# Optimization experiments

Measured on AMD Instinct MI355X. Metric: run time of the kernel, lower is better.

The kernel has to match this reference:

```python
import jax, jax.numpy as jnp
import numpy as np

K = 8
EPS = 1e-8


def setup_inputs() -> dict:
    key = jax.random.key(0)
    tokens = jax.random.normal(key, (32, 1024, 256), dtype=jnp.float32)
    return {"tokens": tokens}


def reference(tokens) -> jnp.ndarray:
    # tokens: [B, N, D] -> adjacency [B, N, N] float32 (0/1), mutual kNN, no self-loops
    B, N, D = tokens.shape
    tn = tokens / (jnp.linalg.norm(tokens, axis=-1, keepdims=True) + EPS)
    sim = jnp.einsum('bnd,bmd->bnm', tn, tn)  # [B, N, N] cosine similarity
    # mask diagonal (add_self=False)
    diag = jnp.eye(N, dtype=bool)
    sim = jnp.where(diag[None, :, :], -jnp.inf, sim)
    k = min(K, N - 1)
    _, topk_idx = jax.lax.top_k(sim, k)  # [B, N, k]
    b_idx = jnp.arange(B)[:, None, None]
    r_idx = jnp.arange(N)[None, :, None]
    adj = jnp.zeros((B, N, N), dtype=bool).at[b_idx, r_idx, topk_idx].set(True)
    # mutual kNN: keep edge only if both directions selected
    adj = adj & jnp.swapaxes(adj, 1, 2)
    return adj.astype(jnp.float32)
```

## Files before the change

### kernel.cpp

```cpp
#include <hip/hip_runtime.h>
#include <math.h>
#include <stdint.h>

#define B_ 32
#define N_ 1024
#define D_ 256
#define K_ 8
#define CAND 12

typedef unsigned short u16;
typedef unsigned int u32;
typedef __attribute__((ext_vector_type(8))) short s16x8;
typedef __attribute__((ext_vector_type(16))) float f32x16;

__device__ inline void cp16(const void* g, void* l) {
    __builtin_amdgcn_global_load_lds((const __attribute__((address_space(1))) void*)g,
                                     (__attribute__((address_space(3))) void*)l, 16, 0, 0);
}

__device__ inline u16 f2bf(float f) {
    uint32_t u = __float_as_uint(f);
    return (u16)((u + 0x7fffu + ((u >> 16) & 1u)) >> 16);
}
__device__ inline u32 umax32(u32 a, u32 b) { return a > b ? a : b; }
__device__ inline u32 umin32(u32 a, u32 b) { return a < b ? a : b; }

__global__ __launch_bounds__(256) void prep_kernel(const float* __restrict__ tok,
                                                   double* __restrict__ invn,
                                                   u16* __restrict__ xhi) {
    const int tid = threadIdx.x;
    const int wave = tid >> 6, lane = tid & 63;
    const int row = blockIdx.x * 4 + wave;
    const float4 v = *reinterpret_cast<const float4*>(tok + (size_t)row * D_ + lane * 4);
    double s = (double)v.x * v.x + (double)v.y * v.y +
               (double)v.z * v.z + (double)v.w * v.w;
    #pragma unroll
    for (int off = 32; off > 0; off >>= 1) s += __shfl_xor(s, off, 64);
    const double inv = 1.0 / (sqrt(s) + 1e-8);
    if (lane == 0) invn[row] = inv;
    ushort4 h;
    h.x = f2bf((float)(v.x * inv));
    h.y = f2bf((float)(v.y * inv));
    h.z = f2bf((float)(v.z * inv));
    h.w = f2bf((float)(v.w * inv));
    *reinterpret_cast<ushort4*>(xhi + (size_t)row * D_ + lane * 4) = h;
}

__global__ __launch_bounds__(256, 4) void sim_topk_kernel(const u16* __restrict__ Xhi,
                                                          u32* __restrict__ candk,
                                                          int* __restrict__ candj) {
    __shared__ __align__(16) char smem[32768];
    u32* keysL = (u32*)smem;

    const int id    = blockIdx.x;
    const int chunk = id >> 3;
    const int b   = (id & 7) * 4 + (chunk >> 5);
    const int rem = chunk & 31;
    const int i0  = (rem >> 1) * 64;
    const int jh  = rem & 1;

    const int tid = threadIdx.x;
    const int w = tid >> 6, lane = tid & 63;
    const int mq = w >> 1, nq = w & 1;
    const int half = lane >> 5;
    const int il = lane & 31;

    const u16* XhiB = Xhi + (size_t)b * N_ * D_;

    const int srr = lane >> 3, spp = lane & 7;
    const int sgoff = (spp ^ srr) * 8;
    char* const wbase = smem + w * 8192;

    const int x7 = il & 7;
    int loff[4];
    #pragma unroll
    for (int ks = 0; ks < 4; ++ks) loff[ks] = il * 128 + (((ks * 2 + half) ^ x7) * 16);

    auto STAGE_A = [&](int kc, int bufn) {
        #pragma unroll
        for (int t = 0; t < 4; ++t)
            cp16(XhiB + (size_t)(i0 + mq * 32 + t * 8 + srr) * D_ + kc * 64 + sgoff,
                 wbase + bufn * 4096 + t * 1024);
    };
    auto STAGE_B = [&](int round, int bufn) {
        const int j0n = (jh * 8 + (round >> 2)) * 64;
        const int kcn = round & 3;
        #pragma unroll
        for (int t = 0; t < 4; ++t)
            cp16(XhiB + (size_t)(j0n + nq * 32 + t * 8 + srr) * D_ + kcn * 64 + sgoff,
                 wbase + bufn * 4096 + t * 1024);
    };

    s16x8 Ahf[4][4];
    STAGE_A(0, 0);
    STAGE_A(1, 1);
    #pragma unroll
    for (int kc = 0; kc < 4; ++kc) {
        asm volatile("s_waitcnt vmcnt(4)" ::: "memory");
        __builtin_amdgcn_sched_barrier(0);
        const char* ab = wbase + (kc & 1) * 4096;
        #pragma unroll
        for (int ks = 0; ks < 4; ++ks)
            Ahf[kc][ks] = *(const s16x8*)(ab + loff[ks]);
        asm volatile("s_waitcnt lgkmcnt(0)" ::: "memory");
        __builtin_amdgcn_sched_barrier(0);
        if (kc < 2) STAGE_A(kc + 2, kc & 1);
        else        STAGE_B(kc - 2, kc & 1);
    }

    const int diag_jt = i0 >> 6;
    u32 keys[CAND];
    #pragma unroll
    for (int c = 0; c < CAND; ++c) keys[c] = 0u;

    for (int lt = 0; lt < 8; ++lt) {
        const int jt = jh * 8 + lt;
        f32x16 acc;
        #pragma unroll
        for (int c = 0; c < 16; ++c) acc[c] = 0.0f;

        #pragma unroll
        for (int kc = 0; kc < 4; ++kc) {
            const int r = lt * 4 + kc;
            if (r < 31) asm volatile("s_waitcnt vmcnt(4)" ::: "memory");
            else        asm volatile("s_waitcnt vmcnt(0)" ::: "memory");
            __builtin_amdgcn_sched_barrier(0);
            const char* bb = wbase + (r & 1) * 4096;
            s16x8 bh[4];
            #pragma unroll
            for (int ks = 0; ks < 4; ++ks)
                bh[ks] = *(const s16x8*)(bb + loff[ks]);
            asm volatile("s_waitcnt lgkmcnt(0)" ::: "memory");
            __builtin_amdgcn_sched_barrier(0);
            if (r + 2 < 32) STAGE_B(r + 2, r & 1);
            #pragma unroll
            for (int ks = 0; ks < 4; ++ks)
                acc = __builtin_amdgcn_mfma_f32_32x32x16_bf16(bh[ks], Ahf[kc][ks], acc, 0, 0, 0);
        }

        const u32 codebase = (u32)(jt << 4);
        const bool diag = (jt == diag_jt) && (mq == nq);
        #pragma unroll
        for (int rg = 0; rg < 16; ++rg) {
            const u32 u = __float_as_uint(acc[rg]);
            const u32 mono = u ^ ((u32)(((int)u) >> 31) | 0x80000000u);
            u32 key = (mono & 0xFFFFFF00u) | (codebase + (u32)rg);
            if (diag && ((rg & 3) + 8 * (rg >> 2) + 4 * half == il)) key = 0u;
            u32 t = key;
            #pragma unroll
            for (int c = 0; c < CAND; ++c) {
                const u32 hi = umax32(keys[c], t);
                t = umin32(keys[c], t);
                keys[c] = hi;
            }
        }
    }

    __syncthreads();
    {
        const int r = mq * 32 + il;
        const int s = nq * 2 + half;
        u32* dst = keysL + (r * 4 + s) * CAND;
        #pragma unroll
        for (int c = 0; c < CAND; ++c) dst[c] = keys[c];
    }
    __syncthreads();

    if (tid < 64) {
        const u32* kl = keysL + tid * (4 * CAND);
        const size_t base = ((size_t)(b * N_ + i0 + tid) * 2 + jh) * CAND;
        int p0 = 0, p1 = 0, p2 = 0, p3 = 0;
        #pragma unroll
        for (int o = 0; o < CAND; ++o) {
            const u32 k0v = kl[p0];
            const u32 k1v = kl[CAND + p1];
            const u32 k2v = kl[2 * CAND + p2];
            const u32 k3v = kl[3 * CAND + p3];
            int bg = 0; u32 bv = k0v;
            if (k1v > bv) { bv = k1v; bg = 1; }
            if (k2v > bv) { bv = k2v; bg = 2; }
            if (k3v > bv) { bv = k3v; bg = 3; }
            const int code = (int)(bv & 0xFFu);
            const int jtv = code >> 4, rg = code & 15;
            candk[base + o] = bv;
            candj[base + o] = jtv * 64 + (bg >> 1) * 32 + (rg & 3) + 8 * (rg >> 2)
                              + 4 * (bg & 1);
            p0 += (bg == 0); p1 += (bg == 1); p2 += (bg == 2); p3 += (bg == 3);
        }
    }
}

__global__ __launch_bounds__(512) void merge_rescore_kernel(const u32* __restrict__ candk,
                                                            const int* __restrict__ candj,
                                                            const float* __restrict__ tok,
                                                            const double* __restrict__ invn,
                                                            int* __restrict__ topk) {
    __shared__ int    mj[32 * CAND];
    __shared__ double dv[32 * CAND];
    const int tid = threadIdx.x;

    const int id    = blockIdx.x;
    const int chunk = id >> 3;
    const int b     = (id & 7) * 4 + (chunk >> 5);
    const int i0    = (chunk & 31) * 32;
    const int R0    = b * N_ + i0;

    if (tid < 32) {
        const size_t base = (size_t)(R0 + tid) * 2 * CAND;
        int p0 = 0, p1 = 0;
        #pragma unroll
        for (int o = 0; o < CAND; ++o) {
            const u32 k0 = candk[base + p0];
            const u32 k1 = candk[base + CAND + p1];
            if (k0 >= k1) { mj[tid * CAND + o] = candj[base + p0];        ++p0; }
            else          { mj[tid * CAND + o] = candj[base + CAND + p1]; ++p1; }
        }
    }
    __syncthreads();

    {
        const int q = tid >> 2, ql = tid & 3;
        const int r = q >> 2;
        const float* qi = tok + (size_t)(R0 + r) * D_;
        const double di = invn[R0 + r];
        #pragma unroll 1
        for (int rr = 0; rr < 3; ++rr) {
            const int c = (q & 3) * 3 + rr;
            const int j = mj[r * CAND + c];
            const float* qj = tok + (size_t)(b * N_ + j) * D_;
            double s = 0.0;
            #pragma unroll 4
            for (int k = 0; k < 16; ++k) {
                const float4 x = *reinterpret_cast<const float4*>(qi + k * 16 + ql * 4);
                const float4 y = *reinterpret_cast<const float4*>(qj + k * 16 + ql * 4);
                s += (double)x.x * y.x + (double)x.y * y.y +
                     (double)x.z * y.z + (double)x.w * y.w;
            }
            s += __shfl_xor(s, 1, 64);
            s += __shfl_xor(s, 2, 64);
            if (ql == 0) dv[r * CAND + c] = s * di * invn[b * N_ + j];
        }
    }
    __syncthreads();

    if (tid < 32) {
        const int out_base = (R0 + tid) * K_;
        #pragma unroll 1
        for (int c = 0; c < CAND; ++c) {
            const double dc = dv[tid * CAND + c]; const int jc = mj[tid * CAND + c];
            int rank = 0;
            #pragma unroll 1
            for (int c2 = 0; c2 < CAND; ++c2) {
                if (c2 == c) continue;
                const double d2 = dv[tid * CAND + c2]; const int j2 = mj[tid * CAND + c2];
                if (d2 > dc || (d2 == dc && j2 < jc)) ++rank;
            }
            if (rank < K_) topk[out_base + rank] = jc;
        }
    }
}

__global__ __launch_bounds__(256) void mutual_kernel(const int* __restrict__ topk,
                                                     float* __restrict__ out) {
    const int gid = blockIdx.x * 256 + threadIdx.x;
    const int row = gid >> 3, s = gid & 7;
    const int j = topk[row * K_ + s];
    const int i = row & (N_ - 1);
    const int* tj = topk + ((row & ~(N_ - 1)) + j) * K_;
    bool m = false;
    #pragma unroll
    for (int u = 0; u < K_; ++u) m = m || (tj[u] == i);
    if (m) out[(size_t)row * N_ + j] = 1.0f;
}

extern "C" void kernel_launch(void* const* d_in, const int* in_sizes, int n_in,
                              void* d_out, int out_size, void* d_ws, size_t ws_size,
                              hipStream_t stream) {
    const float* tok = (const float*)d_in[0];
    float* out = (float*)d_out;
    double* invn = (double*)d_ws;
    int* topk = (int*)((char*)d_ws + (size_t)B_ * N_ * sizeof(double));
    u16* xhi = (u16*)d_out;
    u32* candk = (u32*)((char*)d_out + (size_t)32 * 1024 * 1024);
    int* candj = (int*)((char*)d_out + (size_t)35 * 1024 * 1024);

    prep_kernel<<<dim3(B_ * N_ / 4), 256, 0, stream>>>(tok, invn, xhi);
    sim_topk_kernel<<<dim3(1024), 256, 0, stream>>>(xhi, candk, candj);
    merge_rescore_kernel<<<dim3(B_ * N_ / 32), 512, 0, stream>>>(candk, candj, tok, invn, topk);
    hipMemsetAsync(d_out, 0, (size_t)B_ * N_ * N_ * sizeof(float), stream);
    mutual_kernel<<<dim3(B_ * N_ * K_ / 256), 256, 0, stream>>>(topk, out);
}
```

Before: 259.1 us.

## Fuse output zeroing into mutual kernel and stage query rows in LDS

The mutual kernel now writes every output row in full, one wavefront per row. Each wavefront computes the mutual mask with a ballot and emits float4 zeros and ones, so the separate memset of the 128MB output is no longer needed. The merge/rescore kernel also copies each block's 32 query rows into padded shared memory instead of re-reading them from global memory, and adds a min-blocks launch bound. The cost is an extra 33KB of LDS per block, which may limit occupancy of that kernel.

```diff
diff --git a/kernel.cpp b/kernel.cpp
--- a/kernel.cpp
+++ b/kernel.cpp
@@ -190,11 +190,12 @@
     }
 }
 
-__global__ __launch_bounds__(512) void merge_rescore_kernel(const u32* __restrict__ candk,
-                                                            const int* __restrict__ candj,
-                                                            const float* __restrict__ tok,
-                                                            const double* __restrict__ invn,
-                                                            int* __restrict__ topk) {
+__global__ __launch_bounds__(512, 4) void merge_rescore_kernel(const u32* __restrict__ candk,
+                                                               const int* __restrict__ candj,
+                                                               const float* __restrict__ tok,
+                                                               const double* __restrict__ invn,
+                                                               int* __restrict__ topk) {
+    __shared__ float  qiL[32 * 260];
     __shared__ int    mj[32 * CAND];
     __shared__ double dv[32 * CAND];
     const int tid = threadIdx.x;
@@ -205,6 +206,15 @@
     const int i0    = (chunk & 31) * 32;
     const int R0    = b * N_ + i0;
 
+    {
+        const float4* src = reinterpret_cast<const float4*>(tok + (size_t)R0 * D_);
+        #pragma unroll
+        for (int p = 0; p < 4; ++p) {
+            const int v4 = p * 512 + tid;
+            const int r = v4 >> 6, cc = v4 & 63;
+            *reinterpret_cast<float4*>(&qiL[r * 260 + cc * 4]) = src[v4];
+        }
+    }
     if (tid < 32) {
         const size_t base = (size_t)(R0 + tid) * 2 * CAND;
         int p0 = 0, p1 = 0;
@@ -221,7 +231,7 @@
     {
         const int q = tid >> 2, ql = tid & 3;
         const int r = q >> 2;
-        const float* qi = tok + (size_t)(R0 + r) * D_;
+        const float* qiR = &qiL[r * 260];
         const double di = invn[R0 + r];
         #pragma unroll 1
         for (int rr = 0; rr < 3; ++rr) {
@@ -231,7 +241,7 @@
             double s = 0.0;
             #pragma unroll 4
             for (int k = 0; k < 16; ++k) {
-                const float4 x = *reinterpret_cast<const float4*>(qi + k * 16 + ql * 4);
+                const float4 x = *reinterpret_cast<const float4*>(qiR + k * 16 + ql * 4);
                 const float4 y = *reinterpret_cast<const float4*>(qj + k * 16 + ql * 4);
                 s += (double)x.x * y.x + (double)x.y * y.y +
                      (double)x.z * y.z + (double)x.w * y.w;
@@ -262,15 +272,40 @@
 
 __global__ __launch_bounds__(256) void mutual_kernel(const int* __restrict__ topk,
                                                      float* __restrict__ out) {
-    const int gid = blockIdx.x * 256 + threadIdx.x;
-    const int row = gid >> 3, s = gid & 7;
-    const int j = topk[row * K_ + s];
-    const int i = row & (N_ - 1);
-    const int* tj = topk + ((row & ~(N_ - 1)) + j) * K_;
-    bool m = false;
-    #pragma unroll
-    for (int u = 0; u < K_; ++u) m = m || (tj[u] == i);
-    if (m) out[(size_t)row * N_ + j] = 1.0f;
+    const int w = threadIdx.x >> 6, lane = threadIdx.x & 63;
+    const int R = blockIdx.x * 4 + w;
+    const int i = R & (N_ - 1);
+    const int bbase = R & ~(N_ - 1);
+
+    int cu = 0; bool mu = false;
+    if (lane < 8) {
+        cu = topk[R * K_ + lane];
+        const int4* tj = reinterpret_cast<const int4*>(topk + (size_t)(bbase + cu) * K_);
+        const int4 t0 = tj[0], t1 = tj[1];
+        mu = (t0.x == i) | (t0.y == i) | (t0.z == i) | (t0.w == i) |
+             (t1.x == i) | (t1.y == i) | (t1.z == i) | (t1.w == i);
+    }
+    const unsigned long long mm = __ballot(mu);
+    int c[8];
+    #pragma unroll
+    for (int u = 0; u < 8; ++u) c[u] = __shfl(cu, u, 64);
+
+    float* orow = out + (size_t)R * N_;
+    #pragma unroll
+    for (int p = 0; p < 4; ++p) {
+        const int lo = p * 256 + lane * 4;
+        float4 f = {0.f, 0.f, 0.f, 0.f};
+        #pragma unroll
+        for (int u = 0; u < 8; ++u) {
+            const int rel = c[u] - lo;
+            const float v = ((mm >> u) & 1ull) ? 1.0f : 0.0f;
+            f.x = (rel == 0) ? v : f.x;
+            f.y = (rel == 1) ? v : f.y;
+            f.z = (rel == 2) ? v : f.z;
+            f.w = (rel == 3) ? v : f.w;
+        }
+        *reinterpret_cast<float4*>(orow + lo) = f;
+    }
 }
 
 extern "C" void kernel_launch(void* const* d_in, const int* in_sizes, int n_in,
@@ -287,6 +322,5 @@
     prep_kernel<<<dim3(B_ * N_ / 4), 256, 0, stream>>>(tok, invn, xhi);
     sim_topk_kernel<<<dim3(1024), 256, 0, stream>>>(xhi, candk, candj);
     merge_rescore_kernel<<<dim3(B_ * N_ / 32), 512, 0, stream>>>(candk, candj, tok, invn, topk);
-    hipMemsetAsync(d_out, 0, (size_t)B_ * N_ * N_ * sizeof(float), stream);
-    mutual_kernel<<<dim3(B_ * N_ * K_ / 256), 256, 0, stream>>>(topk, out);
-}
+    mutual_kernel<<<dim3(B_ * N_ / 4), 256, 0, stream>>>(topk, out);
+}
```

Result: faster. 250.4 us (-3.3%).
